# Performance work log

Hardware: AMD Instinct MI355X
Metric: run time of the kernel (lower is better)

The kernel has to match this reference:

```python
import jax, jax.numpy as jnp
import numpy as np

B, C, J, T, S = 16, 4, 19, 256, 10
D1, D2, DS, O = 64, 64, 128, 64  # embed hidden, embed out, similarity dim, out channels
EPS = 1e-5


def setup_inputs() -> dict:
    key = jax.random.key(0)
    ks = jax.random.split(key, 12)
    sc = 0.05
    return {
        'x': jax.random.normal(ks[0], (B, C, J, T, S), dtype=jnp.float32),
        'gamma': jnp.ones((C * J * T,), dtype=jnp.float32),
        'beta': jnp.zeros((C * J * T,), dtype=jnp.float32),
        'w1': jax.random.normal(ks[1], (D1, C), dtype=jnp.float32) * sc,
        'b1': jax.random.normal(ks[2], (D1,), dtype=jnp.float32) * sc,
        'w2': jax.random.normal(ks[3], (D2, D1), dtype=jnp.float32) * sc,
        'b2': jax.random.normal(ks[4], (D2,), dtype=jnp.float32) * sc,
        'ws1': jax.random.normal(ks[5], (DS, D2), dtype=jnp.float32) * sc,
        'bs1': jax.random.normal(ks[6], (DS,), dtype=jnp.float32) * sc,
        'ws2': jax.random.normal(ks[7], (DS, D2), dtype=jnp.float32) * sc,
        'bs2': jax.random.normal(ks[8], (DS,), dtype=jnp.float32) * sc,
        'W': jax.random.normal(ks[9], (D2, O), dtype=jnp.float32) * sc,
    }


def _bn(x, gamma, beta):
    # BatchNorm1d in training mode on x viewed as (B, C*J*T, S): stats over (batch, step)
    b, c, j, t, s = x.shape
    xf = x.reshape(b, c * j * t, s)
    mean = xf.mean(axis=(0, 2), keepdims=True)
    var = ((xf - mean) ** 2).mean(axis=(0, 2), keepdims=True)
    xn = (xf - mean) * jax.lax.rsqrt(var + EPS)
    xn = xn * gamma[None, :, None] + beta[None, :, None]
    return xn.reshape(b, c, j, t, s)


def _conv1x1(x, w, bias):
    # Conv3d with kernel 1 == channel mix: (B,Cin,J,T,S) x (Cout,Cin)
    y = jnp.einsum('bcjts,oc->bojts', x, w)
    return y + bias[None, :, None, None, None]


def reference(x, gamma, beta, w1, b1, w2, b2, ws1, bs1, ws2, bs2, W):
    # embed: norm -> 1x1 conv -> relu -> 1x1 conv -> relu
    h = _bn(x, gamma, beta)
    h = jax.nn.relu(_conv1x1(h, w1, b1))
    h = jax.nn.relu(_conv1x1(h, w2, b2))  # (B, 64, J, T, S)
    # compute_similarity: learned dense adjacency over joints per (b, s, t)
    s1 = _conv1x1(h, ws1, bs1)  # (B, 128, J, T, S)
    s2 = _conv1x1(h, ws2, bs2)
    logits = jnp.einsum('bcjts,bckts->bstjk', s1, s2)  # (B, S, T, J, J)
    att = jax.nn.softmax(logits, axis=-1)
    # aggregate node features then mix channels with weight (64, O)
    agg = jnp.einsum('bstjk,bckts->bstjc', att, h)  # (B, S, T, J, 64)
    out = jnp.einsum('bstjc,co->bojts', agg, W)  # (B, O, J, T, S)
    return out
```

## Files before the change

### kernel.cpp

```cpp
#include <hip/hip_runtime.h>
#include <hip/hip_bf16.h>

#define B_   16
#define C_   4
#define J_   19
#define T_   256
#define S_   10
#define JT_  4864
#define CJT_ 19456

#define WS_SCALE 0
#define WS_SHIFT 19456
#define WS_Q2    38912
#define WS_F16_BYTE ((38912 + 64) * 4)
#define H_W2 0
#define H_Q  4096
#define H_WT 8192

typedef _Float16 f16;
typedef _Float16 half8 __attribute__((ext_vector_type(8)));
typedef float f32x4 __attribute__((ext_vector_type(4)));

__device__ __forceinline__ float bf2f(__hip_bfloat16 v) { return __bfloat162float(v); }
__device__ __forceinline__ float ldin(const void* p, int i, bool f32) {
    if (f32) return ((const float*)p)[i];
    return bf2f(((const __hip_bfloat16*)p)[i]);
}
__device__ __forceinline__ bool dtype_is_f32(const void* gamma) {
    return ((const unsigned short*)gamma)[0] == 0;
}
__device__ __forceinline__ f32x4 mfma16(half8 a, half8 b, f32x4 c) {
    return __builtin_amdgcn_mfma_f32_16x16x32_f16(a, b, c, 0, 0, 0);
}

extern "C" __global__ __launch_bounds__(256)
void bn_stats_kernel(const void* __restrict__ x, const void* __restrict__ gamma,
                     const void* __restrict__ beta, float* __restrict__ wsf)
{
    const bool f32 = dtype_is_f32(gamma);
    const int wave = threadIdx.x >> 6;
    const int lane = threadIdx.x & 63;
    const int ch = blockIdx.x * 4 + wave;
    const int c = ch / JT_;
    const int rem = ch - c * JT_;
    const int j = rem >> 8;
    const int t = rem & 255;

    float sum = 0.f, sq = 0.f;
    for (int i = lane; i < 160; i += 64) {
        int b = i / 10;
        int s = i - b * 10;
        int idx = (((b * C_ + c) * J_ + j) * T_ + t) * S_ + s;
        float v = ldin(x, idx, f32);
        sum += v; sq += v * v;
    }
#pragma unroll
    for (int off = 32; off > 0; off >>= 1) {
        sum += __shfl_down(sum, off);
        sq  += __shfl_down(sq, off);
    }
    if (lane == 0) {
        float mean = sum * (1.f / 160.f);
        float var  = fmaxf(sq * (1.f / 160.f) - mean * mean, 0.f);
        float scl = ldin(gamma, ch, f32) * rsqrtf(var + 1e-5f);
        wsf[WS_SCALE + ch] = scl;
        wsf[WS_SHIFT + ch] = ldin(beta, ch, f32) - mean * scl;
    }
}

extern "C" __global__ __launch_bounds__(256)
void prep_kernel(const void* __restrict__ w2, const void* __restrict__ ws1,
                 const void* __restrict__ ws2, const void* __restrict__ bs1,
                 const void* __restrict__ Wm, const void* __restrict__ gamma,
                 float* __restrict__ wsf)
{
    const bool f32 = dtype_is_f32(gamma);
    f16* hws = (f16*)((char*)wsf + WS_F16_BYTE);
    int id = blockIdx.x * 256 + threadIdx.x;
    if (id < 4096) {
        int a = id >> 6, b = id & 63;
        float acc = 0.f;
        for (int ds = 0; ds < 128; ++ds)
            acc = fmaf(ldin(ws1, ds * 64 + a, f32), ldin(ws2, ds * 64 + b, f32), acc);
        hws[H_Q + id] = (f16)acc;
    } else if (id < 8192) {
        int i = id - 4096;
        hws[H_W2 + i] = (f16)ldin(w2, i, f32);
    } else if (id < 12288) {
        int i = id - 8192;
        int o = i >> 6, c = i & 63;
        hws[H_WT + i] = (f16)ldin(Wm, c * 64 + o, f32);
    } else if (id < 12352) {
        int b = id - 12288;
        float acc = 0.f;
        for (int ds = 0; ds < 128; ++ds)
            acc = fmaf(ldin(ws2, ds * 64 + b, f32), ldin(bs1, ds, f32), acc);
        wsf[WS_Q2 + b] = acc;
    }
}

#define HR 112
#define HSTR 72
#define WTSTR 168
#define ATSTR 40
#define OBSTR 72

#define A1_OFF 0
#define A2_OFF 21504
#define A3_OFF 37632
#define A4_OFF 53760
#define ARENA_BYTES 61760

extern "C" __global__ __launch_bounds__(256, 2)
void fused_kernel(const void* __restrict__ x,
                  const void* __restrict__ w1, const void* __restrict__ b1,
                  const void* __restrict__ b2, const void* __restrict__ gamma,
                  const float* __restrict__ wsf, void* __restrict__ outv)
{
    const bool f32o = dtype_is_f32(gamma);
    const int tid = threadIdx.x;
    const int lane = tid & 63;
    const int wave = tid >> 6;
    const int l15 = lane & 15;
    const int q4 = lane >> 4;

    const int hw  = blockIdx.x;
    const int bid = (hw & 7) * 1024 + (hw >> 3);
    const int b  = bid >> 9;
    const int t  = (bid >> 1) & 255;
    const int sh = bid & 1;

    __shared__ __align__(16) unsigned char arena[ARENA_BYTES];
    __shared__ __align__(16) float w1f[256];
    __shared__ float b1f[64], b2f[64], q2f[64], vbuf[112];

    f16* h1row  = (f16*)(arena + A1_OFF);
    f16* hWT    = (f16*)(arena + A1_OFF);
    f16* h2row  = (f16*)(arena + A2_OFF);
    f16* outb   = (f16*)(arena + A2_OFF);
    f16* urow   = (f16*)(arena + A3_OFF);
    f16* att    = (f16*)(arena + A3_OFF);
    float* logits = (float*)(arena + A4_OFF);
    float* xnr    = (float*)(arena + A4_OFF);

    const f16* hws = (const f16*)((const char*)wsf + WS_F16_BYTE);

    w1f[tid] = ldin(w1, tid, f32o);
    if (tid < 64) {
        b1f[tid] = ldin(b1, tid, f32o);
        b2f[tid] = ldin(b2, tid, f32o);
        q2f[tid] = wsf[WS_Q2 + tid];
    }
    for (int e = tid; e < 400; e += 256) {
        int R = e >> 2, c = e & 3;
        int sL = R / 20, j = R - sL * 20;
        float val = 0.f;
        if (j < 19) {
            int sg = sh * 5 + sL;
            int xidx = ((b * 4 + c) * 19 + j) * 2560 + t * 10 + sg;
            int ch = (c * 19 + j) * 256 + t;
            val = ldin(x, xidx, f32o) * wsf[WS_SCALE + ch] + wsf[WS_SHIFT + ch];
        }
        xnr[e] = val;
    }
    __syncthreads();

    {
        int d = tid & 63;
        float4 wr = *(const float4*)&w1f[d * 4];
        float bb = b1f[d];
        for (int r = 0; r < 25; ++r) {
            int R = wave * 25 + r;
            float4 xc = *(const float4*)&xnr[R * 4];
            float h = fmaf(xc.x, wr.x, fmaf(xc.y, wr.y, fmaf(xc.z, wr.z, fmaf(xc.w, wr.w, bb))));
            h1row[R * HSTR + d] = (f16)fmaxf(h, 0.f);
        }
    }
    __syncthreads();

#define LDFRAG(base, row0, stride, koff) \
    (*(const half8*)((base) + ((row0) + l15) * (stride) + (koff) + (q4 << 3)))

    {
        int n0 = wave * 16;
        half8 B0 = LDFRAG(hws + H_W2, n0, 64, 0);
        half8 B1 = LDFRAG(hws + H_W2, n0, 64, 32);
        float bias = b2f[n0 + l15];
        for (int m = 0; m < 7; ++m) {
            half8 A0 = LDFRAG(h1row, m * 16, HSTR, 0);
            half8 A1 = LDFRAG(h1row, m * 16, HSTR, 32);
            f32x4 c = {bias, bias, bias, bias};
            c = mfma16(A0, B0, c);
            c = mfma16(A1, B1, c);
#pragma unroll
            for (int i = 0; i < 4; ++i) {
                int r = m * 16 + q4 * 4 + i;
                h2row[r * HSTR + n0 + l15] = (f16)fmaxf(c[i], 0.f);
            }
        }
    }
    __syncthreads();

    {
        int n0 = wave * 16;
        half8 B0 = LDFRAG(hws + H_Q, n0, 64, 0);
        half8 B1 = LDFRAG(hws + H_Q, n0, 64, 32);
        for (int m = 0; m < 7; ++m) {
            half8 A0 = LDFRAG(h2row, m * 16, HSTR, 0);
            half8 A1 = LDFRAG(h2row, m * 16, HSTR, 32);
            f32x4 c = {0.f, 0.f, 0.f, 0.f};
            c = mfma16(A0, B0, c);
            c = mfma16(A1, B1, c);
#pragma unroll
            for (int i = 0; i < 4; ++i) {
                int r = m * 16 + q4 * 4 + i;
                urow[r * HSTR + n0 + l15] = (f16)c[i];
            }
        }
        if (tid < 100) {
            const f16* hr = &h2row[tid * HSTR];
            float acc = 0.f;
#pragma unroll
            for (int g = 0; g < 8; ++g) {
                half8 hv = *(const half8*)&hr[g * 8];
#pragma unroll
                for (int jj = 0; jj < 8; ++jj)
                    acc = fmaf((float)hv[jj], q2f[g * 8 + jj], acc);
            }
            vbuf[tid] = acc;
        }
    }
    __syncthreads();

    {
        for (int e = tid; e < 64 * 5 * 13; e += 256) {
            int o = e / 65, rem = e - o * 65;
            int s = rem / 13, kk = 19 + (rem - s * 13);
            hWT[o * WTSTR + s * 32 + kk] = (f16)0.f;
        }
        int n0 = wave * 16;
        half8 B0 = LDFRAG(hws + H_WT, n0, 64, 0);
        half8 B1 = LDFRAG(hws + H_WT, n0, 64, 32);
        for (int m = 0; m < 7; ++m) {
            half8 A0 = LDFRAG(h2row, m * 16, HSTR, 0);
            half8 A1 = LDFRAG(h2row, m * 16, HSTR, 32);
            f32x4 c = {0.f, 0.f, 0.f, 0.f};
            c = mfma16(A0, B0, c);
            c = mfma16(A1, B1, c);
#pragma unroll
            for (int i = 0; i < 4; ++i) {
                int r = m * 16 + q4 * 4 + i;
                int s = r / 20, j = r - s * 20;
                if (r < 100 && j < 19)
                    hWT[(n0 + l15) * WTSTR + s * 32 + j] = (f16)c[i];
            }
        }
        for (int task = wave; task < 10; task += 4) {
            int s = task >> 1, nt = task & 1;
            int n0g = s * 20 + nt * 16;
            half8 Bb0 = LDFRAG(urow, n0g, HSTR, 0);
            half8 Bb1 = LDFRAG(urow, n0g, HSTR, 32);
            int kloc = nt * 16 + l15;
            bool kval = kloc < 19;
            float vv = vbuf[s * 20 + ((kloc < 19) ? kloc : 0)];
#pragma unroll
            for (int mt = 0; mt < 2; ++mt) {
                int m0 = s * 20 + mt * 16;
                half8 A0 = LDFRAG(h2row, m0, HSTR, 0);
                half8 A1 = LDFRAG(h2row, m0, HSTR, 32);
                f32x4 c = {0.f, 0.f, 0.f, 0.f};
                c = mfma16(A0, Bb0, c);
                c = mfma16(A1, Bb1, c);
#pragma unroll
                for (int i = 0; i < 4; ++i) {
                    int j = mt * 16 + q4 * 4 + i;
                    if (j < 19 && kval)
                        logits[s * 400 + j * 20 + kloc] = c[i] + vv;
                }
            }
        }
    }
    __syncthreads();

    if (tid < 95) {
        int sL = tid / 19, j = tid - sL * 19;
        int R = sL * 20 + j;
        const float4* lp = (const float4*)&logits[sL * 400 + j * 20];
        float4 e0 = lp[0], e1 = lp[1], e2 = lp[2], e3 = lp[3], e4 = lp[4];
        e4.w = -1e30f;
        float m = e0.x;
        m = fmaxf(m, e0.y); m = fmaxf(m, e0.z); m = fmaxf(m, e0.w);
        m = fmaxf(m, e1.x); m = fmaxf(m, e1.y); m = fmaxf(m, e1.z); m = fmaxf(m, e1.w);
        m = fmaxf(m, e2.x); m = fmaxf(m, e2.y); m = fmaxf(m, e2.z); m = fmaxf(m, e2.w);
        m = fmaxf(m, e3.x); m = fmaxf(m, e3.y); m = fmaxf(m, e3.z); m = fmaxf(m, e3.w);
        m = fmaxf(m, e4.x); m = fmaxf(m, e4.y); m = fmaxf(m, e4.z);
        e0.x = __expf(e0.x - m); e0.y = __expf(e0.y - m); e0.z = __expf(e0.z - m); e0.w = __expf(e0.w - m);
        e1.x = __expf(e1.x - m); e1.y = __expf(e1.y - m); e1.z = __expf(e1.z - m); e1.w = __expf(e1.w - m);
        e2.x = __expf(e2.x - m); e2.y = __expf(e2.y - m); e2.z = __expf(e2.z - m); e2.w = __expf(e2.w - m);
        e3.x = __expf(e3.x - m); e3.y = __expf(e3.y - m); e3.z = __expf(e3.z - m); e3.w = __expf(e3.w - m);
        e4.x = __expf(e4.x - m); e4.y = __expf(e4.y - m); e4.z = __expf(e4.z - m);
        float sum = e0.x + e0.y + e0.z + e0.w + e1.x + e1.y + e1.z + e1.w
                  + e2.x + e2.y + e2.z + e2.w + e3.x + e3.y + e3.z + e3.w
                  + e4.x + e4.y + e4.z;
        float rs = 1.f / sum;
        half8 h0 = {(f16)(e0.x * rs), (f16)(e0.y * rs), (f16)(e0.z * rs), (f16)(e0.w * rs),
                    (f16)(e1.x * rs), (f16)(e1.y * rs), (f16)(e1.z * rs), (f16)(e1.w * rs)};
        half8 h1 = {(f16)(e2.x * rs), (f16)(e2.y * rs), (f16)(e2.z * rs), (f16)(e2.w * rs),
                    (f16)(e3.x * rs), (f16)(e3.y * rs), (f16)(e3.z * rs), (f16)(e3.w * rs)};
        half8 h2v = {(f16)(e4.x * rs), (f16)(e4.y * rs), (f16)(e4.z * rs),
                     (f16)0.f, (f16)0.f, (f16)0.f, (f16)0.f, (f16)0.f};
        half8 h3v = {(f16)0.f, (f16)0.f, (f16)0.f, (f16)0.f,
                     (f16)0.f, (f16)0.f, (f16)0.f, (f16)0.f};
        f16* ap = &att[R * ATSTR];
        *(half8*)(ap + 0)  = h0;
        *(half8*)(ap + 8)  = h1;
        *(half8*)(ap + 16) = h2v;
        *(half8*)(ap + 24) = h3v;
    }
    __syncthreads();

    for (int task = wave; task < 20; task += 4) {
        int s = task >> 2, nt = task & 3;
        int o0 = nt * 16;
        half8 Bf = *(const half8*)&hWT[(o0 + l15) * WTSTR + s * 32 + (q4 << 3)];
#pragma unroll
        for (int mt = 0; mt < 2; ++mt) {
            int m0 = s * 20 + mt * 16;
            half8 Af = *(const half8*)&att[(m0 + l15) * ATSTR + (q4 << 3)];
            f32x4 c = {0.f, 0.f, 0.f, 0.f};
            c = mfma16(Af, Bf, c);
#pragma unroll
            for (int i = 0; i < 4; ++i) {
                int j = mt * 16 + q4 * 4 + i;
                if (j < 19)
                    outb[(s * 19 + j) * OBSTR + o0 + l15] = (f16)c[i];
            }
        }
    }
    __syncthreads();

    for (int p = 0; p < 5; ++p) {
        int id = p * 256 + tid;
        if (id < 1216) {
            int o = id / 19, j = id - o * 19;
            int obase = ((b * 64 + o) * 19 + j) * 2560 + t * 10 + sh * 5;
            if (f32o) {
                float* of = (float*)outv;
#pragma unroll
                for (int sl = 0; sl < 5; ++sl)
                    of[obase + sl] = (float)outb[(sl * 19 + j) * OBSTR + o];
            } else {
                __hip_bfloat16* ob = (__hip_bfloat16*)outv;
#pragma unroll
                for (int sl = 0; sl < 5; ++sl)
                    ob[obase + sl] = __float2bfloat16((float)outb[(sl * 19 + j) * OBSTR + o]);
            }
        }
    }
}

extern "C" void kernel_launch(void* const* d_in, const int* in_sizes, int n_in,
                              void* d_out, int out_size, void* d_ws, size_t ws_size,
                              hipStream_t stream)
{
    const void* x     = d_in[0];
    const void* gamma = d_in[1];
    const void* beta  = d_in[2];
    const void* w1    = d_in[3];
    const void* b1    = d_in[4];
    const void* w2    = d_in[5];
    const void* b2    = d_in[6];
    const void* ws1   = d_in[7];
    const void* bs1   = d_in[8];
    const void* ws2   = d_in[9];
    const void* bs2   = d_in[10];
    const void* Wm    = d_in[11];
    float* wsf = (float*)d_ws;

    hipLaunchKernelGGL(bn_stats_kernel, dim3(CJT_ / 4), dim3(256), 0, stream,
                       x, gamma, beta, wsf);
    hipLaunchKernelGGL(prep_kernel, dim3(49), dim3(256), 0, stream,
                       w2, ws1, ws2, bs1, Wm, gamma, wsf);
    hipLaunchKernelGGL(fused_kernel, dim3(B_ * T_ * 2), dim3(256), 0, stream,
                       x, w1, b1, b2, gamma, wsf, d_out);
}
```

Before: 447.4 us.

## Merge BN stats and weight prep into one launch with contiguous loads

Merges the BN statistics kernel and the weight-prep kernel into a single 89-block, 1024-thread launch. The first 76 blocks compute per-channel stats with each thread reading 10 contiguous step values per batch and reducing across batch quarters in shared memory. The remaining blocks do the weight preparation. The output epilogue now gathers 5 values per thread and writes them with one memcpy, in the hope of getting wider stores. This removes one launch and the strided 64-lane gathers, but leaves only 89 blocks, which underuses the GPU on the stats pass.

```diff
diff --git a/kernel.cpp b/kernel.cpp
--- a/kernel.cpp
+++ b/kernel.cpp
@@ -22,6 +22,10 @@
 typedef float f32x4 __attribute__((ext_vector_type(4)));
 
 __device__ __forceinline__ float bf2f(__hip_bfloat16 v) { return __bfloat162float(v); }
+__device__ __forceinline__ float bfbits2f(unsigned short u) {
+    unsigned int w = ((unsigned int)u) << 16;
+    return __builtin_bit_cast(float, w);
+}
 __device__ __forceinline__ float ldin(const void* p, int i, bool f32) {
     if (f32) return ((const float*)p)[i];
     return bf2f(((const __hip_bfloat16*)p)[i]);
@@ -33,50 +37,58 @@
     return __builtin_amdgcn_mfma_f32_16x16x32_f16(a, b, c, 0, 0, 0);
 }
 
-extern "C" __global__ __launch_bounds__(256)
-void bn_stats_kernel(const void* __restrict__ x, const void* __restrict__ gamma,
-                     const void* __restrict__ beta, float* __restrict__ wsf)
+extern "C" __global__ __launch_bounds__(1024)
+void setup_kernel(const void* __restrict__ x, const void* __restrict__ gamma,
+                  const void* __restrict__ beta, const void* __restrict__ w2,
+                  const void* __restrict__ ws1, const void* __restrict__ ws2,
+                  const void* __restrict__ bs1, const void* __restrict__ Wm,
+                  float* __restrict__ wsf)
 {
     const bool f32 = dtype_is_f32(gamma);
-    const int wave = threadIdx.x >> 6;
-    const int lane = threadIdx.x & 63;
-    const int ch = blockIdx.x * 4 + wave;
-    const int c = ch / JT_;
-    const int rem = ch - c * JT_;
-    const int j = rem >> 8;
-    const int t = rem & 255;
-
-    float sum = 0.f, sq = 0.f;
-    for (int i = lane; i < 160; i += 64) {
-        int b = i / 10;
-        int s = i - b * 10;
-        int idx = (((b * C_ + c) * J_ + j) * T_ + t) * S_ + s;
-        float v = ldin(x, idx, f32);
-        sum += v; sq += v * v;
-    }
-#pragma unroll
-    for (int off = 32; off > 0; off >>= 1) {
-        sum += __shfl_down(sum, off);
-        sq  += __shfl_down(sq, off);
-    }
-    if (lane == 0) {
-        float mean = sum * (1.f / 160.f);
-        float var  = fmaxf(sq * (1.f / 160.f) - mean * mean, 0.f);
-        float scl = ldin(gamma, ch, f32) * rsqrtf(var + 1e-5f);
-        wsf[WS_SCALE + ch] = scl;
-        wsf[WS_SHIFT + ch] = ldin(beta, ch, f32) - mean * scl;
-    }
-}
-
-extern "C" __global__ __launch_bounds__(256)
-void prep_kernel(const void* __restrict__ w2, const void* __restrict__ ws1,
-                 const void* __restrict__ ws2, const void* __restrict__ bs1,
-                 const void* __restrict__ Wm, const void* __restrict__ gamma,
-                 float* __restrict__ wsf)
-{
-    const bool f32 = dtype_is_f32(gamma);
+    const int tid = threadIdx.x;
+    __shared__ float redS[4][256], redQ[4][256];
+
+    if (blockIdx.x < 76) {
+        const int cj = blockIdx.x;
+        const int t  = tid & 255;
+        const int bq = tid >> 8;
+        float sum = 0.f, sq = 0.f;
+        for (int bb = 0; bb < 4; ++bb) {
+            int b = bq * 4 + bb;
+            size_t base = ((size_t)(b * 76 + cj)) * 2560 + (size_t)t * 10;
+            float va[10];
+            if (f32) {
+                __builtin_memcpy(va, (const float*)x + base, 40);
+            } else {
+                unsigned short ua[10];
+                __builtin_memcpy(ua, (const unsigned short*)x + base, 20);
+#pragma unroll
+                for (int k = 0; k < 10; ++k) va[k] = bfbits2f(ua[k]);
+            }
+#pragma unroll
+            for (int k = 0; k < 10; ++k) {
+                sum += va[k];
+                sq  = fmaf(va[k], va[k], sq);
+            }
+        }
+        redS[bq][t] = sum;
+        redQ[bq][t] = sq;
+        __syncthreads();
+        if (bq == 0) {
+            sum = redS[0][t] + redS[1][t] + redS[2][t] + redS[3][t];
+            sq  = redQ[0][t] + redQ[1][t] + redQ[2][t] + redQ[3][t];
+            int ch = cj * 256 + t;
+            float mean = sum * (1.f / 160.f);
+            float var  = fmaxf(sq * (1.f / 160.f) - mean * mean, 0.f);
+            float scl = ldin(gamma, ch, f32) * rsqrtf(var + 1e-5f);
+            wsf[WS_SCALE + ch] = scl;
+            wsf[WS_SHIFT + ch] = ldin(beta, ch, f32) - mean * scl;
+        }
+        return;
+    }
+
     f16* hws = (f16*)((char*)wsf + WS_F16_BYTE);
-    int id = blockIdx.x * 256 + threadIdx.x;
+    int id = (blockIdx.x - 76) * 1024 + tid;
     if (id < 4096) {
         int a = id >> 6, b = id & 63;
         float acc = 0.f;
@@ -345,15 +357,19 @@
             int o = id / 19, j = id - o * 19;
             int obase = ((b * 64 + o) * 19 + j) * 2560 + t * 10 + sh * 5;
             if (f32o) {
-                float* of = (float*)outv;
+                float tmp[5];
 #pragma unroll
                 for (int sl = 0; sl < 5; ++sl)
-                    of[obase + sl] = (float)outb[(sl * 19 + j) * OBSTR + o];
+                    tmp[sl] = (float)outb[(sl * 19 + j) * OBSTR + o];
+                __builtin_memcpy((float*)outv + obase, tmp, 20);
             } else {
-                __hip_bfloat16* ob = (__hip_bfloat16*)outv;
-#pragma unroll
-                for (int sl = 0; sl < 5; ++sl)
-                    ob[obase + sl] = __float2bfloat16((float)outb[(sl * 19 + j) * OBSTR + o]);
+                unsigned short tmp[5];
+#pragma unroll
+                for (int sl = 0; sl < 5; ++sl) {
+                    __hip_bfloat16 h = __float2bfloat16((float)outb[(sl * 19 + j) * OBSTR + o]);
+                    tmp[sl] = __builtin_bit_cast(unsigned short, h);
+                }
+                __builtin_memcpy((__hip_bfloat16*)outv + obase, tmp, 10);
             }
         }
     }
@@ -377,10 +393,8 @@
     const void* Wm    = d_in[11];
     float* wsf = (float*)d_ws;
 
-    hipLaunchKernelGGL(bn_stats_kernel, dim3(CJT_ / 4), dim3(256), 0, stream,
-                       x, gamma, beta, wsf);
-    hipLaunchKernelGGL(prep_kernel, dim3(49), dim3(256), 0, stream,
-                       w2, ws1, ws2, bs1, Wm, gamma, wsf);
+    hipLaunchKernelGGL(setup_kernel, dim3(89), dim3(1024), 0, stream,
+                       x, gamma, beta, w2, ws1, ws2, bs1, Wm, wsf);
     hipLaunchKernelGGL(fused_kernel, dim3(B_ * T_ * 2), dim3(256), 0, stream,
                        x, w1, b1, b2, gamma, wsf, d_out);
 }
```

New measurement: 436.6 us. 1.02x faster.
